# Kernel tuning notes

Measured on AMD Instinct MI355X. Metric: run time of the kernel, lower is better.

## Reference

```python
import jax, jax.numpy as jnp
import numpy as np

N, IN_DIM, OUT_DIM, HEADS, E = 50000, 256, 256, 4, 800000
HEAD_DIM = OUT_DIM // HEADS
NEG_SLOPE = 0.2


def setup_inputs() -> dict:
    key = jax.random.key(0)
    k = jax.random.split(key, 6)
    h = jax.random.normal(k[0], (N, IN_DIM), dtype=jnp.float32)
    edge_index = jax.random.randint(k[1], (2, E), 0, N, dtype=jnp.int32)
    # xavier-uniform-ish scales
    W = jax.random.normal(k[2], (OUT_DIM, IN_DIM), dtype=jnp.float32) * (1.0 / np.sqrt(IN_DIM))
    b = jnp.zeros((OUT_DIM,), dtype=jnp.float32)
    a_src = jax.random.normal(k[3], (HEADS, HEAD_DIM), dtype=jnp.float32) * (1.0 / np.sqrt(HEAD_DIM))
    a_dst = jax.random.normal(k[4], (HEADS, HEAD_DIM), dtype=jnp.float32) * (1.0 / np.sqrt(HEAD_DIM))
    return {"h": h, "edge_index": edge_index, "W": W, "b": b, "a_src": a_src, "a_dst": a_dst}


def reference(h, edge_index, W, b, a_src, a_dst):
    idx_i, idx_j = edge_index[0], edge_index[1]
    Wh = (h @ W.T + b).reshape(N, HEADS, HEAD_DIM)  # [N,H,D]
    # per-node attention logits components (avoids gathering full Wh per edge twice)
    alpha_src = jnp.einsum('nhd,hd->nh', Wh, a_src)  # [N,H]
    alpha_dst = jnp.einsum('nhd,hd->nh', Wh, a_dst)  # [N,H]
    e = jax.nn.leaky_relu(alpha_src[idx_i] + alpha_dst[idx_j], NEG_SLOPE)  # [E,H]
    # segment softmax over neighbors j of each destination row i (sparse.softmax dim=1)
    m = jax.ops.segment_max(e, idx_i, num_segments=N)  # [N,H]
    ex = jnp.exp(e - m[idx_i])
    denom = jax.ops.segment_sum(ex, idx_i, num_segments=N)  # [N,H]
    att = ex / denom[idx_i]  # [E,H]
    # sparse-mm aggregation: out_i = sum_j att_ij * Wh_j, per head
    out = jax.ops.segment_sum(att[:, :, None] * Wh[idx_j], idx_i, num_segments=N)  # [N,H,D]
    return out.reshape(N, OUT_DIM)
```

## Files before the change

### kernel.cpp

```cpp
#include <hip/hip_runtime.h>
#include <hip/hip_bf16.h>
#include <stdint.h>

constexpr int IN_DIM  = 256;
constexpr int OUT_DIM = 256;
constexpr int HEADS   = 4;
constexpr int HEAD_DIM = 64;
constexpr float NEG_SLOPE = 0.2f;

typedef __attribute__((ext_vector_type(8))) short bf16x8;
typedef __attribute__((ext_vector_type(4))) float f32x4;

static __device__ __forceinline__ unsigned short f2bf(float f) {
  union { float f; uint32_t u; } v; v.f = f;
  uint32_t u = v.u;
  return (unsigned short)((u + 0x7fffu + ((u >> 16) & 1u)) >> 16);
}

__global__ __launch_bounds__(256) void k_prep(
    const float* __restrict__ W, const float* __restrict__ b,
    const float* __restrict__ a_src, const float* __restrict__ a_dst,
    float* __restrict__ csrc, unsigned short* __restrict__ Wb,
    int* __restrict__ counts, int* __restrict__ cursor, int N) {
  int bid = blockIdx.x, t = threadIdx.x;
  int i = bid * 256 + t;
  if (i < N) { counts[i] = 0; cursor[i] = 0; }
  if (bid == 0 && t < 8) {
    int hh = t & 3;
    const float* a = (t < 4 ? a_src : a_dst) + hh * HEAD_DIM;
    float cs = 0.f;
    for (int d = 0; d < HEAD_DIM; ++d) cs += b[hh * HEAD_DIM + d] * a[d];
    csrc[t] = cs;
  } else if (bid >= 8 && bid < 40) {
    int base = (bid - 8) * 2048 + t * 8;
    float4 f0 = *(const float4*)(W + base);
    float4 f1 = *(const float4*)(W + base + 4);
    union { unsigned short us[8]; uint4 u4; } pk;
    pk.us[0]=f2bf(f0.x); pk.us[1]=f2bf(f0.y); pk.us[2]=f2bf(f0.z); pk.us[3]=f2bf(f0.w);
    pk.us[4]=f2bf(f1.x); pk.us[5]=f2bf(f1.y); pk.us[6]=f2bf(f1.z); pk.us[7]=f2bf(f1.w);
    *(uint4*)(Wb + base) = pk.u4;
  }
}

__global__ __launch_bounds__(256) void k_gemm_mfma(
    const float* __restrict__ h, const unsigned short* __restrict__ Wb,
    const float* __restrict__ b,
    const float* __restrict__ a_src, const float* __restrict__ a_dst,
    const float* __restrict__ csrc,
    unsigned short* __restrict__ Wh,
    float* __restrict__ asrc, float* __restrict__ adst, int N) {
  __shared__ unsigned short lds[2 * 20480];
  const int t = threadIdx.x;
  const int w = t >> 6, l = t & 63;
  const int lm = l & 15, g = l >> 4;
  const int r0 = blockIdx.x * 64;

  f32x4 acc[4][4];
  const f32x4 fz = {0.f, 0.f, 0.f, 0.f};
#pragma unroll
  for (int fm = 0; fm < 4; ++fm)
#pragma unroll
    for (int fn = 0; fn < 4; ++fn) acc[fm][fn] = fz;

  float breg[4], asg[4], adg[4];
#pragma unroll
  for (int fn = 0; fn < 4; ++fn) {
    breg[fn] = b[w * 64 + fn * 16 + lm];
    asg[fn]  = a_src[w * 64 + fn * 16 + lm];
    adg[fn]  = a_dst[w * 64 + fn * 16 + lm];
  }

  auto stageA = [&](int ch, int s) {
    int k0 = ch * 64;
    int row = t >> 2;
    int grow = r0 + row;
    unsigned short* dstbase = lds + s * 20480 + row * 64;
#pragma unroll
    for (int cc = 0; cc < 2; ++cc) {
      int c = (t & 3) * 2 + cc;
      union { unsigned short us[8]; bf16x8 v; } pk;
      if (grow < N) {
        const float* src = h + (size_t)grow * 256 + k0 + c * 8;
        float4 f0 = *(const float4*)(src);
        float4 f1 = *(const float4*)(src + 4);
        pk.us[0]=f2bf(f0.x); pk.us[1]=f2bf(f0.y); pk.us[2]=f2bf(f0.z); pk.us[3]=f2bf(f0.w);
        pk.us[4]=f2bf(f1.x); pk.us[5]=f2bf(f1.y); pk.us[6]=f2bf(f1.z); pk.us[7]=f2bf(f1.w);
      } else {
#pragma unroll
        for (int e = 0; e < 8; ++e) pk.us[e] = 0;
      }
      *(bf16x8*)(dstbase + ((c ^ (row & 7)) * 8)) = pk.v;
    }
  };

  auto stageB = [&](int ch, int s) {
    int k0 = ch * 64;
    unsigned short* Bbase = lds + s * 20480 + 4096;
    int c  = l & 7;
    int rs = l >> 3;
#pragma unroll
    for (int i = 0; i < 8; ++i) {
      int row = w * 64 + i * 8 + rs;
      bf16x8 v = *(const bf16x8*)(Wb + (size_t)row * 256 + k0 + c * 8);
      *(bf16x8*)(Bbase + row * 64 + ((c ^ rs) * 8)) = v;
    }
  };

  auto compute = [&](int s) {
    const unsigned short* A = lds + s * 20480;
    const unsigned short* B = lds + s * 20480 + 4096;
#pragma unroll
    for (int ks = 0; ks < 2; ++ks) {
      bf16x8 af[4], bfr[4];
#pragma unroll
      for (int fm = 0; fm < 4; ++fm) {
        int row = fm * 16 + lm;
        af[fm] = *(const bf16x8*)(A + row * 64 + (((ks * 4 + g) ^ (row & 7)) * 8));
      }
#pragma unroll
      for (int fn = 0; fn < 4; ++fn) {
        int row = w * 64 + fn * 16 + lm;
        bfr[fn] = *(const bf16x8*)(B + row * 64 + (((ks * 4 + g) ^ (row & 7)) * 8));
      }
#pragma unroll
      for (int fm = 0; fm < 4; ++fm)
#pragma unroll
        for (int fn = 0; fn < 4; ++fn)
          acc[fm][fn] = __builtin_amdgcn_mfma_f32_16x16x32_bf16(
              af[fm], bfr[fn], acc[fm][fn], 0, 0, 0);
    }
  };

  stageA(0, 0); stageB(0, 0);
  __syncthreads();
#pragma unroll
  for (int ch = 0; ch < 4; ++ch) {
    int cur = ch & 1;
    if (ch < 3) { stageA(ch + 1, cur ^ 1); stageB(ch + 1, cur ^ 1); }
    compute(cur);
    __syncthreads();
  }

#pragma unroll
  for (int fm = 0; fm < 4; ++fm) {
#pragma unroll
    for (int r = 0; r < 4; ++r) {
      int grow = r0 + fm * 16 + g * 4 + r;
      if (grow < N) {
        size_t rowoff = (size_t)grow * 256;
#pragma unroll
        for (int fn = 0; fn < 4; ++fn) {
          int col = w * 64 + fn * 16 + lm;
          Wh[rowoff + col] = f2bf(acc[fm][fn][r] + breg[fn]);
        }
      }
    }
  }

  float cs = csrc[w], cd = csrc[4 + w];
#pragma unroll
  for (int fm = 0; fm < 4; ++fm) {
#pragma unroll
    for (int r = 0; r < 4; ++r) {
      float ps = acc[fm][0][r] * asg[0] + acc[fm][1][r] * asg[1]
               + acc[fm][2][r] * asg[2] + acc[fm][3][r] * asg[3];
      float pd = acc[fm][0][r] * adg[0] + acc[fm][1][r] * adg[1]
               + acc[fm][2][r] * adg[2] + acc[fm][3][r] * adg[3];
#pragma unroll
      for (int off = 1; off < 16; off <<= 1) {
        ps += __shfl_xor(ps, off, 64);
        pd += __shfl_xor(pd, off, 64);
      }
      if (lm == 0) {
        int grow = r0 + fm * 16 + g * 4 + r;
        if (grow < N) {
          asrc[grow * 4 + w] = ps + cs;
          adst[grow * 4 + w] = pd + cd;
        }
      }
    }
  }
}

__global__ __launch_bounds__(256) void k_hist(const int* __restrict__ idx_i,
                                              int* __restrict__ counts, int E) {
  int e = blockIdx.x * 256 + threadIdx.x;
  if (e < E) atomicAdd(&counts[idx_i[e]], 1);
}

__global__ __launch_bounds__(256) void k_scanA(const int* __restrict__ counts,
                                               int* __restrict__ offsets,
                                               int* __restrict__ bsum, int N) {
  __shared__ int s[256];
  int t = threadIdx.x;
  int idx = blockIdx.x * 256 + t;
  int v = (idx < N) ? counts[idx] : 0;
  s[t] = v;
  __syncthreads();
  for (int off = 1; off < 256; off <<= 1) {
    int x = (t >= off) ? s[t - off] : 0;
    __syncthreads();
    s[t] += x;
    __syncthreads();
  }
  if (idx < N) offsets[idx] = s[t] - v;
  if (t == 255) bsum[blockIdx.x] = s[255];
}

__global__ __launch_bounds__(256) void k_scanB(int* __restrict__ bsum, int nb) {
  __shared__ int s[256];
  int t = threadIdx.x;
  int v = (t < nb) ? bsum[t] : 0;
  s[t] = v;
  __syncthreads();
  for (int off = 1; off < 256; off <<= 1) {
    int x = (t >= off) ? s[t - off] : 0;
    __syncthreads();
    s[t] += x;
    __syncthreads();
  }
  if (t < nb) bsum[t] = s[t] - v;
}

__global__ __launch_bounds__(256) void k_scanC(int* __restrict__ offsets,
                                               const int* __restrict__ bsum,
                                               int N, int E) {
  int idx = blockIdx.x * 256 + threadIdx.x;
  if (idx < N) offsets[idx] += bsum[blockIdx.x];
  if (idx == 0) offsets[N] = E;
}

__global__ __launch_bounds__(256) void k_scatter(const int* __restrict__ idx_i,
                                                 const int* __restrict__ idx_j,
                                                 const int* __restrict__ offsets,
                                                 int* __restrict__ cursor,
                                                 int* __restrict__ csr_j, int E) {
  int e = blockIdx.x * 256 + threadIdx.x;
  if (e < E) {
    int i = idx_i[e];
    int p = offsets[i] + atomicAdd(&cursor[i], 1);
    csr_j[p] = idx_j[e];
  }
}

__global__ __launch_bounds__(256) void k_aggregate(const int* __restrict__ offsets,
                                                   const int* __restrict__ csr_j,
                                                   const float* __restrict__ asrc,
                                                   const float* __restrict__ adst,
                                                   const unsigned short* __restrict__ Wh,
                                                   float* __restrict__ out, int N) {
  int t = threadIdx.x;
  int wv = t >> 6, l = t & 63;
  int half = l >> 5, ll = l & 31;
  int i = blockIdx.x * 8 + wv * 2 + half;
  bool valid = i < N;
  int beg = valid ? offsets[i] : 0;
  int end = valid ? offsets[i + 1] : 0;
  int deg = end - beg;
  int hh = ll >> 3;
  float aih = valid ? asrc[i * 4 + hh] : 0.f;

  float o[8];
#pragma unroll
  for (int d = 0; d < 8; ++d) o[d] = 0.f;
  float denom = 0.f;

  for (int q = 0; q < deg; q += 8) {
    int jj[8];
    float wgt[8];
    uint4 vv[8];
#pragma unroll
    for (int k = 0; k < 8; ++k) {
      int qk = q + k;
      int qc = qk < deg - 1 ? qk : deg - 1;
      jj[k] = csr_j[beg + qc];
    }
#pragma unroll
    for (int k = 0; k < 8; ++k) {
      float s = aih + adst[(size_t)jj[k] * 4 + hh];
      s = s > 0.f ? s : NEG_SLOPE * s;
      s = (q + k < deg) ? s : -1e38f;
      wgt[k] = __expf(s);
      vv[k] = *(const uint4*)(Wh + (size_t)jj[k] * 256 + ll * 8);
    }
    denom += ((wgt[0] + wgt[1]) + (wgt[2] + wgt[3])) +
             ((wgt[4] + wgt[5]) + (wgt[6] + wgt[7]));
#pragma unroll
    for (int k = 0; k < 8; ++k) {
      union { uint32_t u; float f; } c0, c1, c2, c3, c4, c5, c6, c7;
      c0.u = vv[k].x << 16; c1.u = vv[k].x & 0xffff0000u;
      c2.u = vv[k].y << 16; c3.u = vv[k].y & 0xffff0000u;
      c4.u = vv[k].z << 16; c5.u = vv[k].z & 0xffff0000u;
      c6.u = vv[k].w << 16; c7.u = vv[k].w & 0xffff0000u;
      float wk = wgt[k];
      o[0] += wk * c0.f; o[1] += wk * c1.f;
      o[2] += wk * c2.f; o[3] += wk * c3.f;
      o[4] += wk * c4.f; o[5] += wk * c5.f;
      o[6] += wk * c6.f; o[7] += wk * c7.f;
    }
  }

  if (valid) {
    float inv = (deg > 0) ? 1.f / denom : 0.f;
    float4 o0 = {o[0] * inv, o[1] * inv, o[2] * inv, o[3] * inv};
    float4 o1 = {o[4] * inv, o[5] * inv, o[6] * inv, o[7] * inv};
    float* dst = out + (size_t)i * 256 + ll * 8;
    *(float4*)(dst) = o0;
    *(float4*)(dst + 4) = o1;
  }
}

extern "C" void kernel_launch(void* const* d_in, const int* in_sizes, int n_in,
                              void* d_out, int out_size, void* d_ws, size_t ws_size,
                              hipStream_t stream) {
  const float* h     = (const float*)d_in[0];
  const int*   eidx  = (const int*)  d_in[1];
  const float* W     = (const float*)d_in[2];
  const float* b     = (const float*)d_in[3];
  const float* a_src = (const float*)d_in[4];
  const float* a_dst = (const float*)d_in[5];
  float* out = (float*)d_out;

  const int N = in_sizes[0] / IN_DIM;
  const int E = in_sizes[1] / 2;
  const int* idx_i = eidx;
  const int* idx_j = eidx + E;

  char* p = (char*)d_ws;
  auto alloc = [&](size_t bytes) {
    char* r = p;
    p += (bytes + 255) & ~(size_t)255;
    return r;
  };
  float* csrc = (float*)alloc(8 * sizeof(float));
  unsigned short* Wb = (unsigned short*)alloc((size_t)OUT_DIM * IN_DIM * sizeof(unsigned short));
  unsigned short* Wh = (unsigned short*)alloc((size_t)N * OUT_DIM * sizeof(unsigned short));
  float* asrc = (float*)alloc((size_t)N * HEADS * sizeof(float));
  float* adst = (float*)alloc((size_t)N * HEADS * sizeof(float));
  int* counts  = (int*)alloc((size_t)N * sizeof(int));
  int* offsets = (int*)alloc(((size_t)N + 1) * sizeof(int));
  int* cursor  = (int*)alloc((size_t)N * sizeof(int));
  int* bsum    = (int*)alloc(256 * sizeof(int));
  int* csrj    = (int*)alloc((size_t)E * sizeof(int));

  const int nbN = (N + 255) / 256;
  const int nbE = (E + 255) / 256;

  k_prep<<<nbN, 256, 0, stream>>>(W, b, a_src, a_dst, csrc, Wb, counts, cursor, N);
  k_gemm_mfma<<<(N + 63) / 64, 256, 0, stream>>>(h, Wb, b, a_src, a_dst, csrc,
                                                 Wh, asrc, adst, N);
  k_hist<<<nbE, 256, 0, stream>>>(idx_i, counts, E);
  k_scanA<<<nbN, 256, 0, stream>>>(counts, offsets, bsum, N);
  k_scanB<<<1, 256, 0, stream>>>(bsum, nbN);
  k_scanC<<<nbN, 256, 0, stream>>>(offsets, bsum, N, E);
  k_scatter<<<nbE, 256, 0, stream>>>(idx_i, idx_j, offsets, cursor, csrj, E);
  k_aggregate<<<(N + 7) / 8, 256, 0, stream>>>(offsets, csrj, asrc, adst, Wh, out, N);
}
```

Measured before the change: 187.2 us.

## Read W fragments from global in GEMM, fuse scan stages, widen aggregate lanes

The GEMM no longer stages W into LDS and instead loads B fragments directly from global/L2 into registers, which shrinks LDS use and should raise occupancy at the cost of uncoalesced global reads. The second and third scan kernels are merged: every block redoes the small block-sum scan in LDS and applies its own prefix, saving one launch. The aggregation kernel now uses 16 lanes per node, each handling 16 output columns with two 16-byte loads, instead of 32 lanes with 8 columns each. This cuts redundant per-edge index and logit loads but processes edges four at a time with less parallelism per node.

```diff
diff --git a/kernel.cpp b/kernel.cpp
--- a/kernel.cpp
+++ b/kernel.cpp
@@ -49,7 +49,7 @@
     const float* __restrict__ csrc,
     unsigned short* __restrict__ Wh,
     float* __restrict__ asrc, float* __restrict__ adst, int N) {
-  __shared__ unsigned short lds[2 * 20480];
+  __shared__ unsigned short lds[2 * 4096];
   const int t = threadIdx.x;
   const int w = t >> 6, l = t & 63;
   const int lm = l & 15, g = l >> 4;
@@ -74,7 +74,7 @@
     int k0 = ch * 64;
     int row = t >> 2;
     int grow = r0 + row;
-    unsigned short* dstbase = lds + s * 20480 + row * 64;
+    unsigned short* dstbase = lds + s * 4096 + row * 64;
 #pragma unroll
     for (int cc = 0; cc < 2; ++cc) {
       int c = (t & 3) * 2 + cc;
@@ -93,51 +93,40 @@
     }
   };
 
-  auto stageB = [&](int ch, int s) {
+  auto compute = [&](int ch, int s) {
     int k0 = ch * 64;
-    unsigned short* Bbase = lds + s * 20480 + 4096;
-    int c  = l & 7;
-    int rs = l >> 3;
-#pragma unroll
-    for (int i = 0; i < 8; ++i) {
-      int row = w * 64 + i * 8 + rs;
-      bf16x8 v = *(const bf16x8*)(Wb + (size_t)row * 256 + k0 + c * 8);
-      *(bf16x8*)(Bbase + row * 64 + ((c ^ rs) * 8)) = v;
-    }
-  };
-
-  auto compute = [&](int s) {
-    const unsigned short* A = lds + s * 20480;
-    const unsigned short* B = lds + s * 20480 + 4096;
+    const unsigned short* A = lds + s * 4096;
+    bf16x8 bfr[2][4];
+#pragma unroll
+    for (int ks = 0; ks < 2; ++ks)
+#pragma unroll
+      for (int fn = 0; fn < 4; ++fn) {
+        int row = w * 64 + fn * 16 + lm;
+        bfr[ks][fn] = *(const bf16x8*)(Wb + (size_t)row * 256 + k0 + (ks * 4 + g) * 8);
+      }
 #pragma unroll
     for (int ks = 0; ks < 2; ++ks) {
-      bf16x8 af[4], bfr[4];
+      bf16x8 af[4];
 #pragma unroll
       for (int fm = 0; fm < 4; ++fm) {
         int row = fm * 16 + lm;
         af[fm] = *(const bf16x8*)(A + row * 64 + (((ks * 4 + g) ^ (row & 7)) * 8));
       }
 #pragma unroll
-      for (int fn = 0; fn < 4; ++fn) {
-        int row = w * 64 + fn * 16 + lm;
-        bfr[fn] = *(const bf16x8*)(B + row * 64 + (((ks * 4 + g) ^ (row & 7)) * 8));
-      }
-#pragma unroll
       for (int fm = 0; fm < 4; ++fm)
 #pragma unroll
         for (int fn = 0; fn < 4; ++fn)
           acc[fm][fn] = __builtin_amdgcn_mfma_f32_16x16x32_bf16(
-              af[fm], bfr[fn], acc[fm][fn], 0, 0, 0);
+              af[fm], bfr[ks][fn], acc[fm][fn], 0, 0, 0);
     }
   };
 
-  stageA(0, 0); stageB(0, 0);
+  stageA(0, 0);
   __syncthreads();
 #pragma unroll
   for (int ch = 0; ch < 4; ++ch) {
-    int cur = ch & 1;
-    if (ch < 3) { stageA(ch + 1, cur ^ 1); stageB(ch + 1, cur ^ 1); }
-    compute(cur);
+    if (ch < 3) stageA(ch + 1, (ch + 1) & 1);
+    compute(ch, ch & 1);
     __syncthreads();
   }
 
@@ -207,7 +196,9 @@
   if (t == 255) bsum[blockIdx.x] = s[255];
 }
 
-__global__ __launch_bounds__(256) void k_scanB(int* __restrict__ bsum, int nb) {
+__global__ __launch_bounds__(256) void k_scanBC(int* __restrict__ offsets,
+                                                const int* __restrict__ bsum,
+                                                int nb, int N, int E) {
   __shared__ int s[256];
   int t = threadIdx.x;
   int v = (t < nb) ? bsum[t] : 0;
@@ -219,14 +210,10 @@
     s[t] += x;
     __syncthreads();
   }
-  if (t < nb) bsum[t] = s[t] - v;
-}
-
-__global__ __launch_bounds__(256) void k_scanC(int* __restrict__ offsets,
-                                               const int* __restrict__ bsum,
-                                               int N, int E) {
-  int idx = blockIdx.x * 256 + threadIdx.x;
-  if (idx < N) offsets[idx] += bsum[blockIdx.x];
+  int bid = blockIdx.x;
+  int add = (bid > 0) ? s[bid - 1] : 0;
+  int idx = bid * 256 + t;
+  if (idx < N) offsets[idx] += add;
   if (idx == 0) offsets[N] = E;
 }
 
@@ -250,63 +237,67 @@
                                                    const unsigned short* __restrict__ Wh,
                                                    float* __restrict__ out, int N) {
   int t = threadIdx.x;
-  int wv = t >> 6, l = t & 63;
-  int half = l >> 5, ll = l & 31;
-  int i = blockIdx.x * 8 + wv * 2 + half;
+  int grp = t >> 4;
+  int ll  = t & 15;
+  int i = blockIdx.x * 16 + grp;
   bool valid = i < N;
   int beg = valid ? offsets[i] : 0;
   int end = valid ? offsets[i + 1] : 0;
   int deg = end - beg;
-  int hh = ll >> 3;
+  int hh = ll >> 2;
   float aih = valid ? asrc[i * 4 + hh] : 0.f;
 
-  float o[8];
-#pragma unroll
-  for (int d = 0; d < 8; ++d) o[d] = 0.f;
+  float o[16];
+#pragma unroll
+  for (int d = 0; d < 16; ++d) o[d] = 0.f;
   float denom = 0.f;
 
-  for (int q = 0; q < deg; q += 8) {
-    int jj[8];
-    float wgt[8];
-    uint4 vv[8];
-#pragma unroll
-    for (int k = 0; k < 8; ++k) {
+  for (int q = 0; q < deg; q += 4) {
+    int jj[4];
+    float wgt[4];
+    uint4 v0[4], v1[4];
+#pragma unroll
+    for (int k = 0; k < 4; ++k) {
       int qk = q + k;
       int qc = qk < deg - 1 ? qk : deg - 1;
       jj[k] = csr_j[beg + qc];
     }
 #pragma unroll
-    for (int k = 0; k < 8; ++k) {
+    for (int k = 0; k < 4; ++k) {
       float s = aih + adst[(size_t)jj[k] * 4 + hh];
       s = s > 0.f ? s : NEG_SLOPE * s;
       s = (q + k < deg) ? s : -1e38f;
       wgt[k] = __expf(s);
-      vv[k] = *(const uint4*)(Wh + (size_t)jj[k] * 256 + ll * 8);
-    }
-    denom += ((wgt[0] + wgt[1]) + (wgt[2] + wgt[3])) +
-             ((wgt[4] + wgt[5]) + (wgt[6] + wgt[7]));
-#pragma unroll
-    for (int k = 0; k < 8; ++k) {
-      union { uint32_t u; float f; } c0, c1, c2, c3, c4, c5, c6, c7;
-      c0.u = vv[k].x << 16; c1.u = vv[k].x & 0xffff0000u;
-      c2.u = vv[k].y << 16; c3.u = vv[k].y & 0xffff0000u;
-      c4.u = vv[k].z << 16; c5.u = vv[k].z & 0xffff0000u;
-      c6.u = vv[k].w << 16; c7.u = vv[k].w & 0xffff0000u;
+      const uint4* src = (const uint4*)(Wh + (size_t)jj[k] * 256 + ll * 16);
+      v0[k] = src[0];
+      v1[k] = src[1];
+    }
+    denom += (wgt[0] + wgt[1]) + (wgt[2] + wgt[3]);
+#pragma unroll
+    for (int k = 0; k < 4; ++k) {
       float wk = wgt[k];
-      o[0] += wk * c0.f; o[1] += wk * c1.f;
-      o[2] += wk * c2.f; o[3] += wk * c3.f;
-      o[4] += wk * c4.f; o[5] += wk * c5.f;
-      o[6] += wk * c6.f; o[7] += wk * c7.f;
+      union { uint32_t u; float f; } c;
+#pragma unroll
+      for (int dw = 0; dw < 4; ++dw) {
+        uint32_t u0 = (&v0[k].x)[dw];
+        c.u = u0 << 16;          o[dw * 2 + 0] += wk * c.f;
+        c.u = u0 & 0xffff0000u;  o[dw * 2 + 1] += wk * c.f;
+        uint32_t u1 = (&v1[k].x)[dw];
+        c.u = u1 << 16;          o[8 + dw * 2 + 0] += wk * c.f;
+        c.u = u1 & 0xffff0000u;  o[8 + dw * 2 + 1] += wk * c.f;
+      }
     }
   }
 
   if (valid) {
     float inv = (deg > 0) ? 1.f / denom : 0.f;
-    float4 o0 = {o[0] * inv, o[1] * inv, o[2] * inv, o[3] * inv};
-    float4 o1 = {o[4] * inv, o[5] * inv, o[6] * inv, o[7] * inv};
-    float* dst = out + (size_t)i * 256 + ll * 8;
-    *(float4*)(dst) = o0;
-    *(float4*)(dst + 4) = o1;
+    float* dst = out + (size_t)i * 256 + ll * 16;
+#pragma unroll
+    for (int f4 = 0; f4 < 4; ++f4) {
+      float4 ov = {o[f4 * 4 + 0] * inv, o[f4 * 4 + 1] * inv,
+                   o[f4 * 4 + 2] * inv, o[f4 * 4 + 3] * inv};
+      *(float4*)(dst + f4 * 4) = ov;
+    }
   }
 }
 
@@ -351,8 +342,7 @@
                                                  Wh, asrc, adst, N);
   k_hist<<<nbE, 256, 0, stream>>>(idx_i, counts, E);
   k_scanA<<<nbN, 256, 0, stream>>>(counts, offsets, bsum, N);
-  k_scanB<<<1, 256, 0, stream>>>(bsum, nbN);
-  k_scanC<<<nbN, 256, 0, stream>>>(offsets, bsum, N, E);
+  k_scanBC<<<nbN, 256, 0, stream>>>(offsets, bsum, nbN, N, E);
   k_scatter<<<nbE, 256, 0, stream>>>(idx_i, idx_j, offsets, cursor, csrj, E);
-  k_aggregate<<<(N + 7) / 8, 256, 0, stream>>>(offsets, csrj, asrc, adst, Wh, out, N);
-}
+  k_aggregate<<<(N + 15) / 16, 256, 0, stream>>>(offsets, csrj, asrc, adst, Wh, out, N);
+}
```

After: 201.3 us. 7.5% more time.
